# Kernel optimization log

Measured on AMD Instinct MI355X. Metric: run time of the kernel, lower is better.

Reference implementation:

```python
import jax, jax.numpy as jnp
import numpy as np

B, T, M, D = 2, 2048, 2048, 128
H = M // D
ROTARY_BASE = 10000
NORM_EPS = 1e-6
QK_SCALE = 1.0 / D  # mult = sqrt(qk_scale) applied to both q and k
INFTY_APPROX = 1e30


def setup_inputs() -> dict:
    key = jax.random.key(0)
    ks = jax.random.split(key, 6)
    w_scale = M ** (-0.5)
    return {
        "x": jax.random.normal(ks[0], (B, T, M), jnp.float32),
        "wq": jax.random.normal(ks[1], (M, H, D), jnp.float32) * w_scale,
        "wk": jax.random.normal(ks[2], (M, H, D), jnp.float32) * w_scale,
        "wv": jax.random.normal(ks[3], (M, H, D), jnp.float32) * w_scale,
        "wo": jax.random.normal(ks[4], (H, D, M), jnp.float32) * w_scale,
        "gq": jnp.zeros((H, 1, D), jnp.float32),
        "bq": jnp.zeros((H, 1, D), jnp.float32),
        "gk": jnp.zeros((H, 1, D), jnp.float32),
        "bk": jnp.zeros((H, 1, D), jnp.float32),
    }


def _qk_layernorm(x, g, b):
    # x: [B,H,T,D]; g,b: [H,1,D]; centered RMS norm with trainable (1+g), b
    x = x - jnp.mean(x, axis=-1, keepdims=True)
    x = x / jnp.sqrt(jnp.mean(jnp.square(x), axis=-1, keepdims=True) + NORM_EPS)
    return x * (1.0 + g)[None] + b[None]


def _rotary(x):
    # x: [B,H,T,D]; half-split rotary encoding
    half = D // 2
    positions = jnp.arange(T, dtype=jnp.float32)[:, None]          # [T,1]
    ang_freqs = jnp.power(float(ROTARY_BASE), -jnp.arange(half, dtype=jnp.float32) / half)[None, :]  # [1,half]
    radians = positions * ang_freqs                                  # [T,half]
    cos = jnp.cos(radians)[None, None].astype(x.dtype)               # [1,1,T,half]
    sin = jnp.sin(radians)[None, None].astype(x.dtype)
    even, odd = jnp.split(x, 2, axis=-1)
    return jnp.concatenate([even * cos - odd * sin, even * sin + odd * cos], axis=-1)


def reference(x, wq, wk, wv, wo, gq, bq, gk, bk):
    q = jnp.einsum('bim,mhd->bhid', x, wq)
    k = jnp.einsum('bim,mhd->bhid', x, wk)
    v = jnp.einsum('bim,mhd->bhid', x, wv)
    q = _rotary(_qk_layernorm(q, gq, bq))
    k = _rotary(_qk_layernorm(k, gk, bk))
    mult = jnp.asarray(QK_SCALE ** 0.5, dtype=x.dtype)
    s = jnp.einsum('bhid,bhjd->bhij', q * mult, k * mult)            # [B,H,T,T]
    i = jnp.arange(T)[:, None]
    j = jnp.arange(T)[None, :]
    future = (i < j)[None, None]                                      # mask future positions
    s = s - jnp.asarray(INFTY_APPROX, dtype=s.dtype) * future
    p = jax.nn.softmax(s, axis=-1)
    o = jnp.einsum('bhij,bhjd->bhid', p, v)
    return jnp.einsum('bhid,hdm->bim', o, wo)
```

## Files before the change

### kernel.cpp

```cpp
#include <hip/hip_runtime.h>


#define NB 2
#define NT 2048
#define NM 2048
#define NH 16
#define ND 128

typedef __attribute__((ext_vector_type(4))) float f32x4;
typedef __attribute__((ext_vector_type(8))) short bf16x8;
typedef __attribute__((ext_vector_type(4))) short bf16x4;

#define AS1 __attribute__((address_space(1)))
#define AS3 __attribute__((address_space(3)))

__device__ __forceinline__ unsigned short f2bf(float f){
  unsigned int u = __float_as_uint(f);
  u = (u + 0x7fffu + ((u >> 16) & 1u)) >> 16;
  return (unsigned short)u;
}
__device__ __forceinline__ float bf2f(short s){
  return __uint_as_float(((unsigned int)(unsigned short)s) << 16);
}
__device__ __forceinline__ float wredsum(float v){
  #pragma unroll
  for (int m = 1; m < 64; m <<= 1) v += __shfl_xor(v, m);
  return v;
}
__device__ __forceinline__ void gload_lds16(const void* g, void* l){
  __builtin_amdgcn_global_load_lds((const AS1 void*)g, (AS3 void*)l, 16, 0, 0);
}

__global__ __launch_bounds__(256) void prep_k(const float* __restrict__ x,
                                              const float* __restrict__ wq,
                                              const float* __restrict__ wk,
                                              const float* __restrict__ wv,
                                              const float* __restrict__ wo,
                                              short* __restrict__ xb,
                                              short* __restrict__ wT,
                                              float* __restrict__ ctab,
                                              float* __restrict__ stab){
  __shared__ float tl[32][33];
  const int bid = blockIdx.x, tid = threadIdx.x;
  if (bid < 8192){
    size_t gid = (size_t)bid * 256 + tid;
    float4 v = *(const float4*)(x + gid * 4);
    bf16x4 o;
    o[0] = (short)f2bf(v.x); o[1] = (short)f2bf(v.y);
    o[2] = (short)f2bf(v.z); o[3] = (short)f2bf(v.w);
    *(bf16x4*)(xb + gid * 4) = o;
  } else if (bid < 24576){
    int tb = bid - 8192;
    int z = tb >> 12, rem = tb & 4095;
    int n0 = (rem & 63) * 32, k0 = (rem >> 6) * 32;
    const float* src = (z == 0) ? wq : (z == 1) ? wk : (z == 2) ? wv : wo;
    short* dst = wT + (size_t)z * 2048 * 2048;
    int cx = tid & 31, ry = tid >> 5;
    #pragma unroll
    for (int p = 0; p < 4; ++p)
      tl[ry + 8 * p][cx] = src[(size_t)(k0 + ry + 8 * p) * 2048 + n0 + cx];
    __syncthreads();
    #pragma unroll
    for (int p = 0; p < 4; ++p)
      dst[(size_t)(n0 + ry + 8 * p) * 2048 + k0 + cx] =
          (short)f2bf(tl[cx][ry + 8 * p]);
  } else {
    int t = (bid - 24576) * 4 + (tid >> 6);
    int i = tid & 63;
    float freq = __expf(-(float)i * (9.210340371976184f / 64.0f));
    float ang = (float)t * freq;
    ctab[t * 64 + i] = cosf(ang);
    stab[t * 64 + i] = sinf(ang);
  }
}

#define NKT 32
__global__ __launch_bounds__(512, 2) void gemm256_k(const short* __restrict__ A,
                                                    const short* __restrict__ Bt,
                                                    short* __restrict__ Cq){
  extern __shared__ char lds[];
  const int tid = threadIdx.x;
  const int wid = tid >> 6, lane = tid & 63;
  const int lrow = lane & 15, g8 = lane >> 4;
  const int wm = wid >> 2, wn = wid & 3;
  const int Kdim = 2048;

  int bid = blockIdx.x;
  int s = (bid & 7) * 48 + (bid >> 3);
  const int bx = s & 15;
  const int by = s >> 4;
  const int m0 = bx * 256, n0 = by * 256;

  const int r8 = lane >> 3;
  const int gcol = ((lane & 7) ^ r8) * 8;
  const short* Ab = A  + (size_t)(m0 + wid * 8 + r8) * Kdim + gcol;
  const short* Bb = Bt + (size_t)(n0 + wid * 8 + r8) * Kdim + gcol;

  f32x4 acc[8][4] = {};

  auto STAGE = [&](int c, int kt){
    #pragma unroll
    for (int h = 0; h < 2; ++h)
      #pragma unroll
      for (int l = 0; l < 2; ++l){
        size_t roff = (size_t)(h * 128 + l * 64) * Kdim + kt * 64;
        char* la = lds + c * 32768 + h * 16384 + l * 8192 + wid * 1024;
        gload_lds16(Ab + roff, la);
        gload_lds16(Bb + roff, la + 65536);
      }
  };
  auto ldA = [&](int c, int mi, int kk) -> bf16x8 {
    int row = mi * 16 + lrow;
    int col = (kk * 64 + g8 * 16) ^ ((lrow & 7) << 4);
    return *(const bf16x8*)(lds + c * 32768 + wm * 16384 + row * 128 + col);
  };
  auto ldB = [&](int c, int ni, int kk) -> bf16x8 {
    int row = (wn & 1) * 64 + ni * 16 + lrow;
    int col = (kk * 64 + g8 * 16) ^ ((lrow & 7) << 4);
    return *(const bf16x8*)(lds + 65536 + c * 32768 + (wn >> 1) * 16384 + row * 128 + col);
  };

  STAGE(0, 0);

  for (int kt = 0; kt < NKT; ++kt){
    const int c = kt & 1;
    asm volatile("s_waitcnt vmcnt(0)" ::: "memory");
    __builtin_amdgcn_s_barrier();
    if (kt + 1 < NKT) STAGE(c ^ 1, kt + 1);

    #pragma unroll
    for (int kk = 0; kk < 2; ++kk){
      bf16x8 bfr[4];
      #pragma unroll
      for (int ni = 0; ni < 4; ++ni) bfr[ni] = ldB(c, ni, kk);
      #pragma unroll
      for (int mh = 0; mh < 2; ++mh){
        bf16x8 afr[4];
        #pragma unroll
        for (int mi = 0; mi < 4; ++mi) afr[mi] = ldA(c, mh * 4 + mi, kk);
        #pragma unroll
        for (int mi = 0; mi < 4; ++mi)
          #pragma unroll
          for (int ni = 0; ni < 4; ++ni)
            acc[mh * 4 + mi][ni] = __builtin_amdgcn_mfma_f32_16x16x32_bf16(
                afr[mi], bfr[ni], acc[mh * 4 + mi][ni], 0, 0, 0);
      }
    }
  }

  const int tsel = by >> 3;
  short* dst = Cq + (size_t)tsel * (NB * NH * NT * ND);
  if (tsel < 2){
    #pragma unroll
    for (int mi = 0; mi < 8; ++mi){
      int rowb = m0 + wm * 128 + mi * 16 + g8 * 4;
      #pragma unroll
      for (int ni = 0; ni < 4; ++ni){
        int col = n0 + wn * 64 + ni * 16 + lrow;
        int hd = col & 2047;
        int hh = hd >> 7, d = hd & 127;
        f32x4 a = acc[mi][ni];
        #pragma unroll
        for (int r = 0; r < 4; ++r){
          int bt = rowb + r;
          int b = bt >> 11, t = bt & 2047;
          dst[(((size_t)(b * NH + hh)) * NT + t) * ND + d] = (short)f2bf(a[r]);
        }
      }
    }
  } else {
    #pragma unroll
    for (int mi = 0; mi < 8; ++mi){
      int rowb = m0 + wm * 128 + mi * 16 + g8 * 4;
      int b = rowb >> 11, t0 = rowb & 2047;
      int jb = t0 >> 6, toff = t0 & 63;
      #pragma unroll
      for (int ni = 0; ni < 4; ++ni){
        int col = n0 + wn * 64 + ni * 16 + lrow;
        int hd = col & 2047;
        int hh = hd >> 7, d = hd & 127;
        f32x4 a = acc[mi][ni];
        bf16x4 w4;
        #pragma unroll
        for (int r = 0; r < 4; ++r) w4[r] = (short)f2bf(a[r]);
        *(bf16x4*)&dst[(((size_t)(b * NH + hh) * 32 + jb) * ND + d) * 64 + toff] = w4;
      }
    }
  }
}

__global__ __launch_bounds__(256) void gemm_bt_k(const short* __restrict__ A,
                                                 const short* __restrict__ Bt,
                                                 float* __restrict__ Cout,
                                                 int Kdim){
  __shared__ short As[2][128 * 32];
  __shared__ short Bs[2][128 * 32];
  const int tid = threadIdx.x;
  const int wid = tid >> 6, lane = tid & 63;
  const int lrow = lane & 15, g8 = lane >> 4;
  const int wm = wid >> 1, wn = wid & 1;
  const int m0 = blockIdx.x * 128, n0 = blockIdx.y * 128;
  f32x4 acc[4][4] = {};
  const int srow = lane >> 2;
  const int skcol = (lane & 3) * 8;

  auto STAGE = [&](int c, int kt){
    #pragma unroll
    for (int i = 0; i < 2; ++i){
      int inst = wid * 2 + i;
      int r = inst * 16 + srow;
      const short* sa = A  + (size_t)(m0 + r) * Kdim + kt + skcol;
      const short* sb = Bt + (size_t)(n0 + r) * Kdim + kt + skcol;
      gload_lds16(sa, (char*)As[c] + inst * 1024);
      gload_lds16(sb, (char*)Bs[c] + inst * 1024);
    }
  };

  STAGE(0, 0);
  const int nkt = Kdim >> 5;
  for (int it = 0; it < nkt; ++it){
    const int c = it & 1;
    asm volatile("s_waitcnt vmcnt(0)" ::: "memory");
    __builtin_amdgcn_s_barrier();
    if (it + 1 < nkt) STAGE(c ^ 1, (it + 1) << 5);

    bf16x8 af[4], bfv[4];
    #pragma unroll
    for (int mi = 0; mi < 4; ++mi)
      af[mi] = *(const bf16x8*)&As[c][(wm * 64 + mi * 16 + lrow) * 32 + g8 * 8];
    #pragma unroll
    for (int ni = 0; ni < 4; ++ni)
      bfv[ni] = *(const bf16x8*)&Bs[c][(wn * 64 + ni * 16 + lrow) * 32 + g8 * 8];
    #pragma unroll
    for (int mi = 0; mi < 4; ++mi)
      #pragma unroll
      for (int ni = 0; ni < 4; ++ni)
        acc[mi][ni] = __builtin_amdgcn_mfma_f32_16x16x32_bf16(
            af[mi], bfv[ni], acc[mi][ni], 0, 0, 0);
  }

  #pragma unroll
  for (int mi = 0; mi < 4; ++mi){
    int rowb = m0 + wm * 64 + mi * 16 + g8 * 4;
    #pragma unroll
    for (int ni = 0; ni < 4; ++ni){
      int col = n0 + wn * 64 + ni * 16 + lrow;
      f32x4 a = acc[mi][ni];
      #pragma unroll
      for (int r = 0; r < 4; ++r)
        Cout[(size_t)(rowb + r) * 2048 + col] = a[r];
    }
  }
}

__global__ __launch_bounds__(256) void norm_rope_k(const short* __restrict__ qkv,
                                                   short* __restrict__ outp,
                                                   const float* __restrict__ gq,
                                                   const float* __restrict__ bq,
                                                   const float* __restrict__ gk,
                                                   const float* __restrict__ bk,
                                                   const float* __restrict__ ctab,
                                                   const float* __restrict__ stab){
  int which = blockIdx.y;
  const short* src = qkv + (size_t)which * (NB * NH * NT * ND);
  short* dst = outp + (size_t)which * (NB * NH * NT * ND);
  const float* g = which ? gk : gq;
  const float* bb = which ? bk : bq;
  const float qs = which ? 1.0f : 0.011271055007f;
  int wid = threadIdx.x >> 6, lane = threadIdx.x & 63;
  size_t row = (size_t)blockIdx.x * 4 + wid;
  int h = (int)((row >> 11) & 15);
  int t = (int)(row & 2047);
  const short* rp = src + row * ND;
  float v0 = bf2f(rp[lane]), v1 = bf2f(rp[lane + 64]);
  float mean = wredsum(v0 + v1) * (1.0f / 128.0f);
  float c0 = v0 - mean, c1 = v1 - mean;
  float ms = wredsum(c0 * c0 + c1 * c1) * (1.0f / 128.0f);
  float rstd = rsqrtf(ms + 1e-6f);
  float n0 = c0 * rstd * (1.0f + g[h * ND + lane]) + bb[h * ND + lane];
  float n1 = c1 * rstd * (1.0f + g[h * ND + lane + 64]) + bb[h * ND + lane + 64];
  float co = ctab[t * 64 + lane], si = stab[t * 64 + lane];
  short* wp = dst + row * ND;
  wp[lane]      = (short)f2bf((n0 * co - n1 * si) * qs);
  wp[lane + 64] = (short)f2bf((n0 * si + n1 * co) * qs);
}

__global__ __launch_bounds__(512) void attn_k(const short* __restrict__ qn,
                                              const short* __restrict__ kn,
                                              const short* __restrict__ vt,
                                              short* __restrict__ ob){
  extern __shared__ char lds[];
  const int tid = threadIdx.x;
  const int wid = tid >> 6, lane = tid & 63;
  const int lrow = lane & 15, g8 = lane >> 4;
  const int id = blockIdx.x;
  const int qs = id >> 5;
  const int bh = id & 31;
  const int b = bh >> 4, h = bh & 15;
  const size_t base = (size_t)bh * NT * ND;
  char* Pw = lds + 98304 + wid * 2048;

  auto STAGE = [&](int jb){
    const int cb = jb % 3;
    #pragma unroll
    for (int i = 0; i < 2; ++i){
      int r0 = wid * 4 + i * 32;
      int r = r0 + (lane >> 4);
      int g = lane & 15;
      gload_lds16(kn + base + (size_t)(jb * 64 + r) * ND + ((g ^ (r & 7)) << 3),
                  lds + cb * 16384 + r0 * 256);
    }
    #pragma unroll
    for (int i = 0; i < 2; ++i){
      int d0 = wid * 8 + i * 64;
      int d = d0 + (lane >> 3);
      int g = lane & 7;
      gload_lds16(vt + base + (size_t)jb * 8192 + d * 64 + ((g ^ (d & 7)) << 3),
                  lds + 49152 + cb * 16384 + d0 * 128);
    }
  };

  for (int pass = 0; pass < 2; ++pass){
    const int qt = pass ? (15 - qs) : qs;
    const int t0 = qt * 128;
    const int wrow0 = t0 + wid * 16;
    const int tq = wrow0 + lrow;
    bf16x8 qf[4];
    #pragma unroll
    for (int dc = 0; dc < 4; ++dc)
      qf[dc] = *(const bf16x8*)(qn + base + (size_t)tq * ND + dc * 32 + g8 * 8);
    f32x4 O[8] = {};
    float m = -3e38f, lsum = 0.0f;
    const int ntiles = 2 * qt + 2;

    __syncthreads();
    STAGE(0);
    STAGE(1);

    for (int jb = 0; jb < ntiles; ++jb){
      if (jb + 1 < ntiles) asm volatile("s_waitcnt vmcnt(4)" ::: "memory");
      else                 asm volatile("s_waitcnt vmcnt(0)" ::: "memory");
      __builtin_amdgcn_s_barrier();
      if (jb + 2 < ntiles) STAGE(jb + 2);
      const char* Kb = lds + (jb % 3) * 16384;
      const char* Vb = lds + 49152 + (jb % 3) * 16384;

      if (jb * 64 <= wrow0 + 15){
        f32x4 st[4] = {};
        __builtin_amdgcn_s_setprio(1);
        #pragma unroll
        for (int dc = 0; dc < 4; ++dc)
          #pragma unroll
          for (int js = 0; js < 4; ++js){
            int jl = js * 16 + lrow;
            bf16x8 kf = *(const bf16x8*)(Kb + jl * 256 +
                          (((dc * 4 + g8) ^ (jl & 7)) << 4));
            st[js] = __builtin_amdgcn_mfma_f32_16x16x32_bf16(kf, qf[dc], st[js], 0, 0, 0);
          }
        __builtin_amdgcn_s_setprio(0);
        if (jb * 64 + 63 > wrow0){
          #pragma unroll
          for (int js = 0; js < 4; ++js)
            #pragma unroll
            for (int r = 0; r < 4; ++r){
              int j = jb * 64 + js * 16 + g8 * 4 + r;
              if (j > tq) st[js][r] = -3e38f;
            }
        }
        f32x4 m4 = st[0];
        #pragma unroll
        for (int js = 1; js < 4; ++js)
          #pragma unroll
          for (int r = 0; r < 4; ++r) m4[r] = fmaxf(m4[r], st[js][r]);
        float mx = fmaxf(fmaxf(m4[0], m4[1]), fmaxf(m4[2], m4[3]));
        mx = fmaxf(mx, __shfl_xor(mx, 16));
        mx = fmaxf(mx, __shfl_xor(mx, 32));
        if (!__all(mx <= m + 8.0f)){
          float mnew = fmaxf(m, mx);
          float fac = exp2f(m - mnew);
          m = mnew;
          lsum *= fac;
          #pragma unroll
          for (int dcb = 0; dcb < 8; ++dcb) O[dcb] *= fac;
        }
        float ps = 0.0f;
        #pragma unroll
        for (int js = 0; js < 4; ++js){
          float p0 = exp2f(st[js][0] - m);
          float p1 = exp2f(st[js][1] - m);
          float p2 = exp2f(st[js][2] - m);
          float p3 = exp2f(st[js][3] - m);
          ps += (p0 + p1) + (p2 + p3);
          unsigned int lo, hi;
          asm("v_cvt_pk_bf16_f32 %0, %1, %2" : "=v"(lo) : "v"(p0), "v"(p1));
          asm("v_cvt_pk_bf16_f32 %0, %1, %2" : "=v"(hi) : "v"(p2), "v"(p3));
          uint2 w; w.x = lo; w.y = hi;
          *(uint2*)(Pw + lrow * 128 + ((js * 32 + g8 * 8) ^ ((lrow & 7) << 4))) = w;
        }
        ps += __shfl_xor(ps, 16);
        ps += __shfl_xor(ps, 32);
        lsum += ps;
        asm volatile("s_waitcnt lgkmcnt(0)" ::: "memory");
        __builtin_amdgcn_s_setprio(1);
        #pragma unroll
        for (int j32 = 0; j32 < 2; ++j32){
          bf16x8 pf = *(const bf16x8*)(Pw + lrow * 128 +
                        ((j32 * 64 + g8 * 16) ^ ((lrow & 7) << 4)));
          #pragma unroll
          for (int dcb = 0; dcb < 8; ++dcb){
            int d = dcb * 16 + lrow;
            bf16x8 vf = *(const bf16x8*)(Vb + d * 128 +
                          (((j32 * 4 + g8) ^ (d & 7)) << 4));
            O[dcb] = __builtin_amdgcn_mfma_f32_16x16x32_bf16(vf, pf, O[dcb], 0, 0, 0);
          }
        }
        __builtin_amdgcn_s_setprio(0);
      }
    }
    float inv = 1.0f / lsum;
    #pragma unroll
    for (int dcb = 0; dcb < 8; ++dcb){
      bf16x4 w4;
      #pragma unroll
      for (int r = 0; r < 4; ++r) w4[r] = (short)f2bf(O[dcb][r] * inv);
      *(bf16x4*)(ob + ((size_t)(b * NT + tq)) * (NH * ND) + h * ND + dcb * 16 + g8 * 4) = w4;
    }
  }
}

extern "C" void kernel_launch(void* const* d_in, const int* in_sizes, int n_in,
                              void* d_out, int out_size, void* d_ws, size_t ws_size,
                              hipStream_t stream){
  const float* x  = (const float*)d_in[0];
  const float* wq = (const float*)d_in[1];
  const float* wk = (const float*)d_in[2];
  const float* wv = (const float*)d_in[3];
  const float* wo = (const float*)d_in[4];
  const float* gq = (const float*)d_in[5];
  const float* bq = (const float*)d_in[6];
  const float* gk = (const float*)d_in[7];
  const float* bk = (const float*)d_in[8];

  char* ws = (char*)d_ws;
  short* xb   = (short*)(ws);
  short* wT   = (short*)(ws + 16777216);
  short* qkvb = (short*)(ws + 50331648);
  short* qkn  = (short*)(ws + 100663296);
  short* ob   = (short*)(ws + 134217728);
  float* ctab = (float*)(ws + 150994944);
  float* stab = (float*)(ws + 151519232);

  (void)hipFuncSetAttribute((const void*)gemm256_k,
                            hipFuncAttributeMaxDynamicSharedMemorySize, 131072);
  (void)hipFuncSetAttribute((const void*)attn_k,
                            hipFuncAttributeMaxDynamicSharedMemorySize, 114688);

  prep_k<<<dim3(25088), dim3(256), 0, stream>>>(x, wq, wk, wv, wo, xb, wT, ctab, stab);
  gemm256_k<<<dim3(384), dim3(512), 131072, stream>>>(xb, wT, qkvb);
  norm_rope_k<<<dim3(16384, 2), dim3(256), 0, stream>>>(qkvb, qkn, gq, bq, gk, bk, ctab, stab);
  attn_k<<<dim3(256), dim3(512), 114688, stream>>>(qkn, qkn + 8388608,
                                                   qkvb + 2 * (size_t)8388608, ob);
  gemm_bt_k<<<dim3(32, 16), dim3(256), 0, stream>>>(ob, wT + 3 * (size_t)4194304,
                                                    (float*)d_out, 2048);
}
```

Before: 277.2 us.

## Shrink QKV GEMM tile to 256x128 with K-step 32 for higher occupancy

Restructures the QKV projection GEMM from 256x256 tiles with a 64-wide K step to 256x128 tiles with a 32-wide K step. This doubles the grid to 768 blocks and cuts LDS per block from 128KB to 48KB, so four blocks can run per CU. The swizzle, the warp layout (4x2 instead of 2x4) and the output indexing are adapted to match. The goal is better CU fill and latency hiding. The cost is lower per-tile data reuse, more global traffic, and twice as many barriers per unit of K.

```diff
diff --git a/kernel.cpp b/kernel.cpp
--- a/kernel.cpp
+++ b/kernel.cpp
@@ -74,86 +74,73 @@
   }
 }
 
-#define NKT 32
-__global__ __launch_bounds__(512, 2) void gemm256_k(const short* __restrict__ A,
+#define NKT2 64
+__global__ __launch_bounds__(512, 4) void gemm256_k(const short* __restrict__ A,
                                                     const short* __restrict__ Bt,
                                                     short* __restrict__ Cq){
   extern __shared__ char lds[];
   const int tid = threadIdx.x;
   const int wid = tid >> 6, lane = tid & 63;
   const int lrow = lane & 15, g8 = lane >> 4;
-  const int wm = wid >> 2, wn = wid & 3;
+  const int wm = wid >> 1, wn = wid & 1;
   const int Kdim = 2048;
 
   int bid = blockIdx.x;
-  int s = (bid & 7) * 48 + (bid >> 3);
+  int s = (bid & 7) * 96 + (bid >> 3);
   const int bx = s & 15;
   const int by = s >> 4;
-  const int m0 = bx * 256, n0 = by * 256;
-
-  const int r8 = lane >> 3;
-  const int gcol = ((lane & 7) ^ r8) * 8;
-  const short* Ab = A  + (size_t)(m0 + wid * 8 + r8) * Kdim + gcol;
-  const short* Bb = Bt + (size_t)(n0 + wid * 8 + r8) * Kdim + gcol;
-
-  f32x4 acc[8][4] = {};
+  const int m0 = bx * 256, n0 = by * 128;
+
+  const int ar = lane >> 2;
+  const int ag = (lane & 3) ^ (ar & 3);
+  const short* Ab = A  + (size_t)(m0 + wid * 32 + ar) * Kdim + ag * 8;
+  const short* Bb = Bt + (size_t)(n0 + wid * 16 + ar) * Kdim + ag * 8;
+
+  f32x4 acc[4][4] = {};
 
   auto STAGE = [&](int c, int kt){
     #pragma unroll
-    for (int h = 0; h < 2; ++h)
-      #pragma unroll
-      for (int l = 0; l < 2; ++l){
-        size_t roff = (size_t)(h * 128 + l * 64) * Kdim + kt * 64;
-        char* la = lds + c * 32768 + h * 16384 + l * 8192 + wid * 1024;
-        gload_lds16(Ab + roff, la);
-        gload_lds16(Bb + roff, la + 65536);
-      }
+    for (int i = 0; i < 2; ++i)
+      gload_lds16(Ab + (size_t)(i * 16) * Kdim + kt * 32,
+                  lds + c * 16384 + wid * 2048 + i * 1024);
+    gload_lds16(Bb + kt * 32, lds + 32768 + c * 8192 + wid * 1024);
   };
-  auto ldA = [&](int c, int mi, int kk) -> bf16x8 {
-    int row = mi * 16 + lrow;
-    int col = (kk * 64 + g8 * 16) ^ ((lrow & 7) << 4);
-    return *(const bf16x8*)(lds + c * 32768 + wm * 16384 + row * 128 + col);
+  auto ldA = [&](int c, int mi) -> bf16x8 {
+    int row = wm * 64 + mi * 16 + lrow;
+    return *(const bf16x8*)(lds + c * 16384 + row * 64 + ((g8 ^ (row & 3)) << 4));
   };
-  auto ldB = [&](int c, int ni, int kk) -> bf16x8 {
-    int row = (wn & 1) * 64 + ni * 16 + lrow;
-    int col = (kk * 64 + g8 * 16) ^ ((lrow & 7) << 4);
-    return *(const bf16x8*)(lds + 65536 + c * 32768 + (wn >> 1) * 16384 + row * 128 + col);
+  auto ldB = [&](int c, int ni) -> bf16x8 {
+    int row = wn * 64 + ni * 16 + lrow;
+    return *(const bf16x8*)(lds + 32768 + c * 8192 + row * 64 + ((g8 ^ (row & 3)) << 4));
   };
 
   STAGE(0, 0);
 
-  for (int kt = 0; kt < NKT; ++kt){
+  for (int kt = 0; kt < NKT2; ++kt){
     const int c = kt & 1;
     asm volatile("s_waitcnt vmcnt(0)" ::: "memory");
     __builtin_amdgcn_s_barrier();
-    if (kt + 1 < NKT) STAGE(c ^ 1, kt + 1);
-
-    #pragma unroll
-    for (int kk = 0; kk < 2; ++kk){
-      bf16x8 bfr[4];
-      #pragma unroll
-      for (int ni = 0; ni < 4; ++ni) bfr[ni] = ldB(c, ni, kk);
-      #pragma unroll
-      for (int mh = 0; mh < 2; ++mh){
-        bf16x8 afr[4];
-        #pragma unroll
-        for (int mi = 0; mi < 4; ++mi) afr[mi] = ldA(c, mh * 4 + mi, kk);
-        #pragma unroll
-        for (int mi = 0; mi < 4; ++mi)
-          #pragma unroll
-          for (int ni = 0; ni < 4; ++ni)
-            acc[mh * 4 + mi][ni] = __builtin_amdgcn_mfma_f32_16x16x32_bf16(
-                afr[mi], bfr[ni], acc[mh * 4 + mi][ni], 0, 0, 0);
-      }
-    }
-  }
-
-  const int tsel = by >> 3;
+    if (kt + 1 < NKT2) STAGE(c ^ 1, kt + 1);
+
+    bf16x8 af[4], bfv[4];
+    #pragma unroll
+    for (int mi = 0; mi < 4; ++mi) af[mi] = ldA(c, mi);
+    #pragma unroll
+    for (int ni = 0; ni < 4; ++ni) bfv[ni] = ldB(c, ni);
+    #pragma unroll
+    for (int mi = 0; mi < 4; ++mi)
+      #pragma unroll
+      for (int ni = 0; ni < 4; ++ni)
+        acc[mi][ni] = __builtin_amdgcn_mfma_f32_16x16x32_bf16(
+            af[mi], bfv[ni], acc[mi][ni], 0, 0, 0);
+  }
+
+  const int tsel = by >> 4;
   short* dst = Cq + (size_t)tsel * (NB * NH * NT * ND);
   if (tsel < 2){
     #pragma unroll
-    for (int mi = 0; mi < 8; ++mi){
-      int rowb = m0 + wm * 128 + mi * 16 + g8 * 4;
+    for (int mi = 0; mi < 4; ++mi){
+      int rowb = m0 + wm * 64 + mi * 16 + g8 * 4;
       #pragma unroll
       for (int ni = 0; ni < 4; ++ni){
         int col = n0 + wn * 64 + ni * 16 + lrow;
@@ -170,8 +157,8 @@
     }
   } else {
     #pragma unroll
-    for (int mi = 0; mi < 8; ++mi){
-      int rowb = m0 + wm * 128 + mi * 16 + g8 * 4;
+    for (int mi = 0; mi < 4; ++mi){
+      int rowb = m0 + wm * 64 + mi * 16 + g8 * 4;
       int b = rowb >> 11, t0 = rowb & 2047;
       int jb = t0 >> 6, toff = t0 & 63;
       #pragma unroll
@@ -451,12 +438,12 @@
   float* stab = (float*)(ws + 151519232);
 
   (void)hipFuncSetAttribute((const void*)gemm256_k,
-                            hipFuncAttributeMaxDynamicSharedMemorySize, 131072);
+                            hipFuncAttributeMaxDynamicSharedMemorySize, 49152);
   (void)hipFuncSetAttribute((const void*)attn_k,
                             hipFuncAttributeMaxDynamicSharedMemorySize, 114688);
 
   prep_k<<<dim3(25088), dim3(256), 0, stream>>>(x, wq, wk, wv, wo, xb, wT, ctab, stab);
-  gemm256_k<<<dim3(384), dim3(512), 131072, stream>>>(xb, wT, qkvb);
+  gemm256_k<<<dim3(768), dim3(512), 49152, stream>>>(xb, wT, qkvb);
   norm_rope_k<<<dim3(16384, 2), dim3(256), 0, stream>>>(qkvb, qkn, gq, bq, gk, bk, ctab, stab);
   attn_k<<<dim3(256), dim3(512), 114688, stream>>>(qkn, qkn + 8388608,
                                                    qkvb + 2 * (size_t)8388608, ob);
```

After: 274.0 us. Within noise of the previous version (-1.2%).
